# Kernel tuning notes

Hardware: AMD Instinct MI355X
Metric: run time of the kernel (lower is better)

## Reference

```python
import jax, jax.numpy as jnp
import numpy as np

N_HEADS = 16
NEG = -1000000000.0  # masked_fill value from the original code


def setup_inputs() -> dict:
    key = jax.random.key(0)
    ks = jax.random.split(key, 7)
    D = 1024
    x = jax.random.normal(ks[0], (2, 2048, D), dtype=jnp.float32)
    s = 1.0 / np.sqrt(D)
    Wq = jax.random.normal(ks[1], (D, D), dtype=jnp.float32) * s
    bq = jax.random.normal(ks[2], (D,), dtype=jnp.float32) * 0.01
    Wk = jax.random.normal(ks[3], (D, D), dtype=jnp.float32) * s
    bk = jax.random.normal(ks[4], (D,), dtype=jnp.float32) * 0.01
    Wv = jax.random.normal(ks[5], (D, D), dtype=jnp.float32) * s
    bv = jax.random.normal(ks[6], (D,), dtype=jnp.float32) * 0.01
    return {"x": x, "Wq": Wq, "bq": bq, "Wk": Wk, "bk": bk, "Wv": Wv, "bv": bv}


def reference(x, Wq, bq, Wk, bk, Wv, bv):
    B, S, D = x.shape
    H = N_HEADS
    dh = D // H
    # nn.Linear: x @ W.T + b
    Q = (x @ Wq.T + bq).reshape(B, S, H, dh)
    K = (x @ Wk.T + bk).reshape(B, S, H, dh)
    V = (x @ Wv.T + bv).reshape(B, S, H, dh)
    # NOTE: original scales by sqrt(n_heads), not sqrt(d_head) -- faithful.
    scale = jnp.asarray(H, x.dtype) ** 0.5
    scores = jnp.einsum('bqhd,bkhd->bhqk', Q, K) / scale  # [B,H,S,S]
    # Original: mask = triu(ones, diag=1); scores.masked_fill(mask == 0, -1e9)
    # i.e. positions where the STRICT-UPPER mask is False (lower triangle incl.
    # diagonal) get -1e9. Faithful reproduction of that (buggy) behavior.
    triu = jnp.triu(jnp.ones((S, S), dtype=bool), k=1)  # [S,S]
    scores = jnp.where(triu[None, None, :, :], scores, jnp.asarray(NEG, x.dtype))
    probs = jax.nn.softmax(scores, axis=-1)
    # dropout is identity at inference
    out = jnp.einsum('bhqk,bkhd->bqhd', probs, V).reshape(B, S, D)
    return out
```

## Files before the change

### kernel.cpp

```cpp
#include <hip/hip_runtime.h>
#include <stdint.h>

typedef unsigned short u16;
typedef __attribute__((ext_vector_type(8))) short bf16x8;
typedef __attribute__((ext_vector_type(4))) float floatx4;

#define MFMA16(a, b, c) __builtin_amdgcn_mfma_f32_16x16x32_bf16(a, b, c, 0, 0, 0)
#define MEMFENCE asm volatile("" ::: "memory")

#if __has_builtin(__builtin_amdgcn_exp2f)
#define EXP2(x) __builtin_amdgcn_exp2f(x)
#else
#define EXP2(x) __expf(0.6931471805599453f * (x))
#endif

__device__ __forceinline__ u16 f2bf(float f) {
  unsigned u = __builtin_bit_cast(unsigned, f);
  return (u16)((u + 0x7FFFu + ((u >> 16) & 1u)) >> 16);
}
__device__ __forceinline__ u16 f2bf_hu(float f) {
  return (u16)((__builtin_bit_cast(unsigned, f) + 0x8000u) >> 16);
}
__device__ __forceinline__ float bf2f(u16 v) {
  return __builtin_bit_cast(float, (unsigned)v << 16);
}

__device__ __forceinline__ void glds16(void* lds, const void* g) {
  __builtin_amdgcn_global_load_lds((const __attribute__((address_space(1))) void*)g,
                                   (__attribute__((address_space(3))) void*)lds,
                                   16, 0, 0);
}

__global__ __launch_bounds__(256) void cvt_all(
    const float* __restrict__ x, const float* __restrict__ w0,
    const float* __restrict__ w1, const float* __restrict__ w2,
    u16* __restrict__ xb, u16* __restrict__ Wb) {
  const int bid = blockIdx.x;
  const float* src;
  u16* dst;
  int i;
  if (bid < 4096) {
    src = x; dst = xb; i = bid * 256 + threadIdx.x;
  } else {
    const int z = (bid - 4096) >> 10;
    src = (z == 0) ? w0 : (z == 1) ? w1 : w2;
    dst = Wb + (size_t)z * (1024 * 1024);
    i = ((bid - 4096) & 1023) * 256 + threadIdx.x;
  }
  float4 f = reinterpret_cast<const float4*>(src)[i];
  ushort4 o;
  o.x = f2bf(f.x); o.y = f2bf(f.y); o.z = f2bf(f.z); o.w = f2bf(f.w);
  reinterpret_cast<ushort4*>(dst)[i] = o;
}

__global__ __launch_bounds__(256, 3) void qkv_gemm(
    const u16* __restrict__ xb, const u16* __restrict__ Wb,
    const float* __restrict__ bq, const float* __restrict__ bk,
    const float* __restrict__ bv,
    u16* __restrict__ Qb, u16* __restrict__ Kb, u16* __restrict__ VTb) {
  __shared__ __attribute__((aligned(16))) u16 smem[2 * 128 * 64];
  u16* As = smem;
  u16* Bs = smem + 128 * 64;

  const int tid = threadIdx.x;
  const int w = tid >> 6, lane = tid & 63;
  const int lo = lane & 15, quad = lane >> 4;
  const int which = blockIdx.z;
  const int m0 = blockIdx.x * 128, n0 = blockIdx.y * 128;

  const u16* W = Wb + (size_t)which * (1024 * 1024);
  const int wm = (w >> 1) * 64, wn = (w & 1) * 64;

  floatx4 acc[4][4];
  for (int i = 0; i < 4; ++i)
    for (int j = 0; j < 4; ++j) acc[i][j] = (floatx4)0.f;

  const int arow = lane >> 3;
  const int aswz = ((lane & 7) ^ arow) * 8;

  for (int kt = 0; kt < 16; ++kt) {
    const int k0 = kt * 64;
    for (int j = 0; j < 4; ++j) {
      const int seg = w * 4 + j;
      glds16(As + seg * 512, xb + (size_t)(m0 + seg * 8 + arow) * 1024 + k0 + aswz);
      glds16(Bs + seg * 512, W + (size_t)(n0 + seg * 8 + arow) * 1024 + k0 + aswz);
    }
    __syncthreads();
    for (int kk = 0; kk < 2; ++kk) {
      const int swz = ((kk * 4 + quad) ^ (lo & 7)) * 8;
      bf16x8 af[4], bfr[4];
      for (int it = 0; it < 4; ++it)
        af[it] = *reinterpret_cast<const bf16x8*>(As + (wm + it * 16 + lo) * 64 + swz);
      for (int jt = 0; jt < 4; ++jt)
        bfr[jt] = *reinterpret_cast<const bf16x8*>(Bs + (wn + jt * 16 + lo) * 64 + swz);
      for (int it = 0; it < 4; ++it)
        for (int jt = 0; jt < 4; ++jt)
          acc[it][jt] = MFMA16(af[it], bfr[jt], acc[it][jt]);
    }
    __syncthreads();
  }

  const float* bias = (which == 0) ? bq : (which == 1) ? bk : bv;
  float bb[4];
  for (int jt = 0; jt < 4; ++jt) bb[jt] = bias[n0 + wn + jt * 16 + lo];
  const int b = m0 >> 11;

  if (which < 2) {
    const float scl = (which == 0) ? 0.36067376022224085f : 1.0f;
    u16* Tw = smem + w * (16 * 72);
    const int hblk = (n0 + wn) >> 6;
    u16* dst = ((which == 0) ? Qb : Kb) +
               ((size_t)(b * 16 + hblk) * 2048 + ((m0 & 2047) + wm)) * 64;
    for (int it = 0; it < 4; ++it) {
      for (int jt = 0; jt < 4; ++jt)
        for (int r = 0; r < 4; ++r) {
          const int m = quad * 4 + r, col = jt * 16 + lo;
          Tw[m * 72 + (((col >> 3) ^ (m & 7)) * 8) + (col & 7)] =
              f2bf((acc[it][jt][r] + bb[jt]) * scl);
        }
      MEMFENCE;
      for (int rd = 0; rd < 2; ++rd) {
        const int sr = rd * 8 + (lane >> 3), d8 = lane & 7;
        bf16x8 v = *reinterpret_cast<const bf16x8*>(Tw + sr * 72 + ((d8 ^ (sr & 7)) * 8));
        *reinterpret_cast<bf16x8*>(dst + (size_t)(it * 16 + sr) * 64 + d8 * 8) = v;
      }
      MEMFENCE;
    }
  } else {
    for (int pass = 0; pass < 2; ++pass) {
      if ((wm >> 6) == pass) {
        for (int it = 0; it < 4; ++it)
          for (int jt = 0; jt < 4; ++jt)
            for (int r = 0; r < 4; ++r) {
              const int n = wn + jt * 16 + lo;
              const int m = it * 16 + quad * 4 + r;
              smem[n * 72 + (((m >> 3) ^ (n & 7)) * 8) + (m & 7)] =
                  f2bf(acc[it][jt][r] + bb[jt]);
            }
      }
      __syncthreads();
      for (int rd = 0; rd < 4; ++rd) {
        const int n = (tid >> 3) + rd * 32, m8 = tid & 7;
        bf16x8 v = *reinterpret_cast<const bf16x8*>(smem + n * 72 + ((m8 ^ (n & 7)) * 8));
        const int ng = n0 + n, h = ng >> 6, d = ng & 63;
        const int s = (m0 & 2047) + pass * 64 + m8 * 8;
        *reinterpret_cast<bf16x8*>(VTb + ((size_t)(b * 16 + h) * 64 + d) * 2048 + s) = v;
      }
      __syncthreads();
    }
  }
}

__global__ __launch_bounds__(256, 2) void attn(
    const u16* __restrict__ Qb, const u16* __restrict__ Kb,
    const u16* __restrict__ VTb, float* __restrict__ out) {
  __shared__ __attribute__((aligned(16))) u16 Ks[2][64 * 64];
  __shared__ __attribute__((aligned(16))) u16 Pt[4][2][16 * 64];

  const int L = blockIdx.x;
  const int bh = L & 31;
  const int s5 = L >> 5;
  const int qs = (s5 < 8) ? s5 : 23 - s5;
  const int kstart = 2 * qs;

  const int tid = threadIdx.x, w = tid >> 6, lane = tid & 63;
  const int lo = lane & 15, quad = lane >> 4;

  const u16* Qh = Qb + (size_t)bh * (2048 * 64);
  const u16* Kh = Kb + (size_t)bh * (2048 * 64);
  const u16* Vh = VTb + (size_t)bh * (64 * 2048);

  int qrow[2];
  bf16x8 qf[2][2];
  for (int s = 0; s < 2; ++s) {
    qrow[s] = qs * 128 + w * 32 + s * 16 + lo;
    qf[s][0] = *reinterpret_cast<const bf16x8*>(Qh + (size_t)qrow[s] * 64 + quad * 8);
    qf[s][1] = *reinterpret_cast<const bf16x8*>(Qh + (size_t)qrow[s] * 64 + 32 + quad * 8);
  }

  float lrun[2] = {0.f, 0.f};
  floatx4 acc[2][4];
  for (int s = 0; s < 2; ++s)
    for (int dt = 0; dt < 4; ++dt) acc[s][dt] = (floatx4)0.f;

  const int srow8 = lane >> 3, sblk = lane & 7;
  const int sswz = (sblk ^ srow8) * 8;

  for (int j = 0; j < 2; ++j) {
    const int b8 = (w * 2 + j) * 8;
    glds16(&Ks[0][b8 * 64], Kh + (size_t)(kstart * 64 + b8 + srow8) * 64 + sswz);
  }
  __syncthreads();

  for (int kt = kstart; kt < 32; ++kt) {
    const int cur = (kt - kstart) & 1, nxt = cur ^ 1;

    const int d2 = kt - 2 * qs;
    const bool skip = (d2 == 0) && (w >= 2);
    const bool maskp = ((d2 == 0) && (w < 2)) || ((d2 == 1) && (w >= 2));

    bf16x8 vfrag[2][4];
    if (!skip) {
      for (int kk = 0; kk < 2; ++kk)
        for (int dt = 0; dt < 4; ++dt)
          vfrag[kk][dt] = *reinterpret_cast<const bf16x8*>(
              Vh + (size_t)(dt * 16 + lo) * 2048 + kt * 64 + kk * 32 + quad * 8);
    }

    if (kt < 31)
      for (int j = 0; j < 2; ++j) {
        const int b8 = (w * 2 + j) * 8;
        glds16(&Ks[nxt][b8 * 64], Kh + (size_t)((kt + 1) * 64 + b8 + srow8) * 64 + sswz);
      }
    const u16* ksb = Ks[cur];

    if (!skip) {
      floatx4 sc[2][4];
      for (int s = 0; s < 2; ++s)
        for (int t = 0; t < 4; ++t) sc[s][t] = (floatx4)0.f;
      __builtin_amdgcn_s_setprio(1);
      for (int kk = 0; kk < 2; ++kk) {
        const int swz = ((kk * 4 + quad) ^ (lo & 7)) * 8;
        for (int t = 0; t < 4; ++t) {
          bf16x8 ka = *reinterpret_cast<const bf16x8*>(ksb + (t * 16 + lo) * 64 + swz);
          sc[0][t] = MFMA16(ka, qf[0][kk], sc[0][t]);
          sc[1][t] = MFMA16(ka, qf[1][kk], sc[1][t]);
        }
      }
      __builtin_amdgcn_s_setprio(0);

      for (int s = 0; s < 2; ++s) {
        u16* ptw = &Pt[w][s][0];
        for (int t = 0; t < 4; ++t) {
          float p0 = EXP2(sc[s][t][0]), p1 = EXP2(sc[s][t][1]);
          float p2 = EXP2(sc[s][t][2]), p3 = EXP2(sc[s][t][3]);
          if (maskp) {
            const int key = kt * 64 + t * 16 + quad * 4;
            p0 = (key + 0 > qrow[s]) ? p0 : 0.f;
            p1 = (key + 1 > qrow[s]) ? p1 : 0.f;
            p2 = (key + 2 > qrow[s]) ? p2 : 0.f;
            p3 = (key + 3 > qrow[s]) ? p3 : 0.f;
          }
          lrun[s] += (p0 + p1) + (p2 + p3);
          ushort4 pk;
          pk.x = f2bf_hu(p0); pk.y = f2bf_hu(p1);
          pk.z = f2bf_hu(p2); pk.w = f2bf_hu(p3);
          u16* pdst = ptw + lo * 64 +
                      (((2 * t + (quad >> 1)) ^ (lo & 7)) * 8) + (quad & 1) * 4;
          *reinterpret_cast<ushort4*>(pdst) = pk;
        }
      }
      MEMFENCE;

      __builtin_amdgcn_s_setprio(1);
      for (int kk = 0; kk < 2; ++kk) {
        const int pswz = ((kk * 4 + quad) ^ (lo & 7)) * 8;
        bf16x8 pb0 = *reinterpret_cast<const bf16x8*>(&Pt[w][0][lo * 64] + pswz);
        bf16x8 pb1 = *reinterpret_cast<const bf16x8*>(&Pt[w][1][lo * 64] + pswz);
        for (int dt = 0; dt < 4; ++dt) {
          acc[0][dt] = MFMA16(vfrag[kk][dt], pb0, acc[0][dt]);
          acc[1][dt] = MFMA16(vfrag[kk][dt], pb1, acc[1][dt]);
        }
      }
      __builtin_amdgcn_s_setprio(0);
      MEMFENCE;
    }
    __syncthreads();
  }

  const int b = bh >> 4, hh = bh & 15;
  for (int s = 0; s < 2; ++s) {
    float l = lrun[s];
    l += __shfl_xor(l, 16);
    l += __shfl_xor(l, 32);
    if (l != 0.f) {
      const float rl = 1.f / l;
      float* op = out + ((size_t)(b * 2048 + qrow[s])) * 1024 + hh * 64 + quad * 4;
      for (int dt = 0; dt < 4; ++dt) {
        float4 o4;
        o4.x = acc[s][dt][0] * rl; o4.y = acc[s][dt][1] * rl;
        o4.z = acc[s][dt][2] * rl; o4.w = acc[s][dt][3] * rl;
        *reinterpret_cast<float4*>(op + dt * 16) = o4;
      }
    }
  }
}

__global__ __launch_bounds__(256) void fix2047(const u16* __restrict__ VTb,
                                               float* __restrict__ out) {
  const int bh = blockIdx.x;
  const u16* Vh = VTb + (size_t)bh * (64 * 2048);
  const int t = threadIdx.x;
  const int d = t >> 2, j = t & 3;
  float s = 0.f;
  const u16* row = Vh + (size_t)d * 2048 + j * 512;
  for (int i = 0; i < 64; ++i) {
    bf16x8 v = *reinterpret_cast<const bf16x8*>(row + i * 8);
    for (int e = 0; e < 8; ++e) s += bf2f((u16)v[e]);
  }
  s += __shfl_xor(s, 1);
  s += __shfl_xor(s, 2);
  if (j == 0) {
    const int b = bh >> 4, h = bh & 15;
    out[((size_t)(b * 2048 + 2047)) * 1024 + h * 64 + d] = s * (1.f / 2048.f);
  }
}

extern "C" void kernel_launch(void* const* d_in, const int* in_sizes, int n_in,
                              void* d_out, int out_size, void* d_ws, size_t ws_size,
                              hipStream_t stream) {
  const float* x  = (const float*)d_in[0];
  const float* Wq = (const float*)d_in[1];
  const float* bq = (const float*)d_in[2];
  const float* Wk = (const float*)d_in[3];
  const float* bk = (const float*)d_in[4];
  const float* Wv = (const float*)d_in[5];
  const float* bv = (const float*)d_in[6];
  float* out = (float*)d_out;

  char* ws = (char*)d_ws;
  u16* xb  = (u16*)(ws);
  u16* Wb  = (u16*)(ws + (8u << 20));
  u16* Qb  = (u16*)(ws + (14u << 20));
  u16* Kb  = (u16*)(ws + (22u << 20));
  u16* VTb = (u16*)(ws + (30u << 20));

  cvt_all<<<7168, 256, 0, stream>>>(x, Wq, Wk, Wv, xb, Wb);
  qkv_gemm<<<dim3(32, 8, 3), 256, 0, stream>>>(xb, Wb, bq, bk, bv, Qb, Kb, VTb);
  attn<<<dim3(512), 256, 0, stream>>>(Qb, Kb, VTb, out);
  fix2047<<<dim3(32), 256, 0, stream>>>(VTb, out);
}
```

Before: 170.0 us.

## Split attention key range in two halves with combine kernel, load K into registers

Each query tile's key range is now split into two halves handled by separate blocks, doubling the grid so the triangular workload spreads over more CUs. Partial accumulators (one half in fp32 written to out, the other in bf16 to workspace) and row sums are merged by a new combine kernel. K fragments now come straight from global memory into registers with a one-tile prefetch, which removes the LDS K buffer and the per-iteration barrier. Occupancy hint goes to 3 blocks. The cost is an extra kernel launch, an extra global round trip for partials, and bf16 rounding of one partial accumulator.

```diff
diff --git a/kernel.cpp b/kernel.cpp
--- a/kernel.cpp
+++ b/kernel.cpp
@@ -151,17 +151,19 @@
   }
 }
 
-__global__ __launch_bounds__(256, 2) void attn(
+__global__ __launch_bounds__(256, 3) void attn(
     const u16* __restrict__ Qb, const u16* __restrict__ Kb,
-    const u16* __restrict__ VTb, float* __restrict__ out) {
-  __shared__ __attribute__((aligned(16))) u16 Ks[2][64 * 64];
+    const u16* __restrict__ VTb, float* __restrict__ out,
+    u16* __restrict__ acc1, float* __restrict__ l0, float* __restrict__ l1) {
   __shared__ __attribute__((aligned(16))) u16 Pt[4][2][16 * 64];
 
-  const int L = blockIdx.x;
-  const int bh = L & 31;
-  const int s5 = L >> 5;
-  const int qs = (s5 < 8) ? s5 : 23 - s5;
-  const int kstart = 2 * qs;
+  const int blk = blockIdx.x;
+  const int bh = blk & 31;
+  const int item = blk >> 5;
+  const int qs = item >> 1, h = item & 1;
+  const int Lh = 16 - qs;
+  const int kstart = 2 * qs + h * Lh;
+  const int kend = kstart + Lh;
 
   const int tid = threadIdx.x, w = tid >> 6, lane = tid & 63;
   const int lo = lane & 15, quad = lane >> 4;
@@ -183,18 +185,15 @@
   for (int s = 0; s < 2; ++s)
     for (int dt = 0; dt < 4; ++dt) acc[s][dt] = (floatx4)0.f;
 
-  const int srow8 = lane >> 3, sblk = lane & 7;
-  const int sswz = (sblk ^ srow8) * 8;
-
-  for (int j = 0; j < 2; ++j) {
-    const int b8 = (w * 2 + j) * 8;
-    glds16(&Ks[0][b8 * 64], Kh + (size_t)(kstart * 64 + b8 + srow8) * 64 + sswz);
-  }
-  __syncthreads();
-
-  for (int kt = kstart; kt < 32; ++kt) {
-    const int cur = (kt - kstart) & 1, nxt = cur ^ 1;
-
+  bf16x8 kfr[8];
+  {
+    const u16* kp = Kh + (size_t)kstart * (64 * 64) + (size_t)lo * 64 + quad * 8;
+    for (int kk = 0; kk < 2; ++kk)
+      for (int t = 0; t < 4; ++t)
+        kfr[kk * 4 + t] = *reinterpret_cast<const bf16x8*>(kp + t * 16 * 64 + kk * 32);
+  }
+
+  for (int kt = kstart; kt < kend; ++kt) {
     const int d2 = kt - 2 * qs;
     const bool skip = (d2 == 0) && (w >= 2);
     const bool maskp = ((d2 == 0) && (w < 2)) || ((d2 == 1) && (w >= 2));
@@ -207,28 +206,26 @@
               Vh + (size_t)(dt * 16 + lo) * 2048 + kt * 64 + kk * 32 + quad * 8);
     }
 
-    if (kt < 31)
-      for (int j = 0; j < 2; ++j) {
-        const int b8 = (w * 2 + j) * 8;
-        glds16(&Ks[nxt][b8 * 64], Kh + (size_t)((kt + 1) * 64 + b8 + srow8) * 64 + sswz);
-      }
-    const u16* ksb = Ks[cur];
-
+    floatx4 sc[2][4];
     if (!skip) {
-      floatx4 sc[2][4];
       for (int s = 0; s < 2; ++s)
         for (int t = 0; t < 4; ++t) sc[s][t] = (floatx4)0.f;
-      __builtin_amdgcn_s_setprio(1);
-      for (int kk = 0; kk < 2; ++kk) {
-        const int swz = ((kk * 4 + quad) ^ (lo & 7)) * 8;
+      for (int kk = 0; kk < 2; ++kk)
         for (int t = 0; t < 4; ++t) {
-          bf16x8 ka = *reinterpret_cast<const bf16x8*>(ksb + (t * 16 + lo) * 64 + swz);
-          sc[0][t] = MFMA16(ka, qf[0][kk], sc[0][t]);
-          sc[1][t] = MFMA16(ka, qf[1][kk], sc[1][t]);
+          sc[0][t] = MFMA16(kfr[kk * 4 + t], qf[0][kk], sc[0][t]);
+          sc[1][t] = MFMA16(kfr[kk * 4 + t], qf[1][kk], sc[1][t]);
         }
-      }
-      __builtin_amdgcn_s_setprio(0);
-
+    }
+
+    {
+      const int ktn = (kt + 1 < kend) ? kt + 1 : kt;
+      const u16* kp = Kh + (size_t)ktn * (64 * 64) + (size_t)lo * 64 + quad * 8;
+      for (int kk = 0; kk < 2; ++kk)
+        for (int t = 0; t < 4; ++t)
+          kfr[kk * 4 + t] = *reinterpret_cast<const bf16x8*>(kp + t * 16 * 64 + kk * 32);
+    }
+
+    if (!skip) {
       for (int s = 0; s < 2; ++s) {
         u16* ptw = &Pt[w][s][0];
         for (int t = 0; t < 4; ++t) {
@@ -252,7 +249,6 @@
       }
       MEMFENCE;
 
-      __builtin_amdgcn_s_setprio(1);
       for (int kk = 0; kk < 2; ++kk) {
         const int pswz = ((kk * 4 + quad) ^ (lo & 7)) * 8;
         bf16x8 pb0 = *reinterpret_cast<const bf16x8*>(&Pt[w][0][lo * 64] + pswz);
@@ -262,10 +258,8 @@
           acc[1][dt] = MFMA16(vfrag[kk][dt], pb1, acc[1][dt]);
         }
       }
-      __builtin_amdgcn_s_setprio(0);
       MEMFENCE;
     }
-    __syncthreads();
   }
 
   const int b = bh >> 4, hh = bh & 15;
@@ -273,17 +267,47 @@
     float l = lrun[s];
     l += __shfl_xor(l, 16);
     l += __shfl_xor(l, 32);
-    if (l != 0.f) {
-      const float rl = 1.f / l;
+    if (h == 0) {
       float* op = out + ((size_t)(b * 2048 + qrow[s])) * 1024 + hh * 64 + quad * 4;
       for (int dt = 0; dt < 4; ++dt) {
         float4 o4;
-        o4.x = acc[s][dt][0] * rl; o4.y = acc[s][dt][1] * rl;
-        o4.z = acc[s][dt][2] * rl; o4.w = acc[s][dt][3] * rl;
+        o4.x = acc[s][dt][0]; o4.y = acc[s][dt][1];
+        o4.z = acc[s][dt][2]; o4.w = acc[s][dt][3];
         *reinterpret_cast<float4*>(op + dt * 16) = o4;
       }
-    }
-  }
+      if (quad == 0) l0[(size_t)bh * 2048 + qrow[s]] = l;
+    } else {
+      u16* ap = acc1 + ((size_t)bh * 2048 + qrow[s]) * 64 + quad * 4;
+      for (int dt = 0; dt < 4; ++dt) {
+        ushort4 a4;
+        a4.x = f2bf(acc[s][dt][0]); a4.y = f2bf(acc[s][dt][1]);
+        a4.z = f2bf(acc[s][dt][2]); a4.w = f2bf(acc[s][dt][3]);
+        *reinterpret_cast<ushort4*>(ap + dt * 16) = a4;
+      }
+      if (quad == 0) l1[(size_t)bh * 2048 + qrow[s]] = l;
+    }
+  }
+}
+
+__global__ __launch_bounds__(256) void combine(
+    float* __restrict__ out, const u16* __restrict__ acc1,
+    const float* __restrict__ l0, const float* __restrict__ l1) {
+  const int R = blockIdx.x;
+  const int c4 = threadIdx.x;
+  const int hd = c4 >> 4;
+  const int b = R >> 11, q = R & 2047;
+  const size_t bhq = (size_t)(b * 16 + hd) * 2048 + q;
+  const float ls = l0[bhq] + l1[bhq];
+  if (ls == 0.f) return;
+  const float rl = 1.f / ls;
+  float4* o4 = reinterpret_cast<float4*>(out) + (size_t)R * 256 + c4;
+  float4 o = *o4;
+  const ushort4 a = reinterpret_cast<const ushort4*>(acc1)[bhq * 16 + (c4 & 15)];
+  o.x = (o.x + bf2f(a.x)) * rl;
+  o.y = (o.y + bf2f(a.y)) * rl;
+  o.z = (o.z + bf2f(a.z)) * rl;
+  o.w = (o.w + bf2f(a.w)) * rl;
+  *o4 = o;
 }
 
 __global__ __launch_bounds__(256) void fix2047(const u16* __restrict__ VTb,
@@ -324,9 +348,13 @@
   u16* Qb  = (u16*)(ws + (14u << 20));
   u16* Kb  = (u16*)(ws + (22u << 20));
   u16* VTb = (u16*)(ws + (30u << 20));
+  u16*   acc1 = (u16*)(ws);
+  float* l0   = (float*)(ws + (8u << 20));
+  float* l1   = (float*)(ws + (8u << 20) + (256u << 10));
 
   cvt_all<<<7168, 256, 0, stream>>>(x, Wq, Wk, Wv, xb, Wb);
   qkv_gemm<<<dim3(32, 8, 3), 256, 0, stream>>>(xb, Wb, bq, bk, bv, Qb, Kb, VTb);
-  attn<<<dim3(512), 256, 0, stream>>>(Qb, Kb, VTb, out);
+  attn<<<dim3(1024), 256, 0, stream>>>(Qb, Kb, VTb, out, acc1, l0, l1);
+  combine<<<dim3(4096), 256, 0, stream>>>(out, acc1, l0, l1);
   fix2047<<<dim3(32), 256, 0, stream>>>(VTb, out);
 }
```

After: 279.0 us. +64.1%, slower.
